# Performance work log

Measured on AMD Instinct MI355X. Metric: run time of the kernel, lower is better.

## Reference

```python
import jax, jax.numpy as jnp
import numpy as np

E, D, H, T = 8, 1024, 2816, 16384


def setup_inputs() -> dict:
    key = jax.random.key(0)
    k1, k2, k3, k4 = jax.random.split(key, 4)
    x = jax.random.normal(k1, (T, D), dtype=jnp.float32)
    # Params sized per init (w1/w3: [E, H, D], w2: [E, D, H]), trunc-normal-ish scale 0.02
    w1 = 0.02 * jax.random.normal(k2, (E, H, D), dtype=jnp.float32)
    w2 = 0.02 * jax.random.normal(k3, (E, D, H), dtype=jnp.float32)
    w3 = 0.02 * jax.random.normal(k4, (E, H, D), dtype=jnp.float32)
    # Per-expert token counts summing to < T (tail rows are padding, output zeros)
    rng = np.random.default_rng(0)
    props = rng.dirichlet(4.0 * np.ones(E))
    counts = np.floor(props * (T - 64)).astype(np.int32)
    num_tokens_per_expert = jnp.asarray(counts, dtype=jnp.int32)
    return {"x": x, "w1": w1, "w2": w2, "w3": w3,
            "num_tokens_per_expert": num_tokens_per_expert}


def reference(x, w1, w2, w3, num_tokens_per_expert):
    # Tokens are grouped contiguously by expert; grouped GEMM via lax.ragged_dot.
    g = num_tokens_per_expert.astype(jnp.int32)
    # rhs for ragged_dot must be [groups, k, n]
    h1 = jax.lax.ragged_dot(x, jnp.swapaxes(w1, 1, 2), g)   # [T, H] = x @ w1[e].T
    h3 = jax.lax.ragged_dot(x, jnp.swapaxes(w3, 1, 2), g)   # [T, H]
    h = jax.nn.silu(h1) * h3                                # SwiGLU
    out = jax.lax.ragged_dot(h, jnp.swapaxes(w2, 1, 2), g)  # [T, D]
    # Rows beyond sum(counts) are padding -> zeros, matching torch vstack of zeros
    valid = jnp.arange(x.shape[0]) < jnp.sum(g)
    return jnp.where(valid[:, None], out, jnp.zeros((), dtype=out.dtype))
```

## Files before the change

### kernel.cpp

```cpp
#include <hip/hip_runtime.h>

#define NE 8
#define DD 1024
#define HH 2816
#define TT 16384
#define MAX_TILES (TT / 128 + NE)

typedef __bf16 bf16;
typedef __bf16 bf16x4 __attribute__((ext_vector_type(4)));
typedef __bf16 bf16x8 __attribute__((ext_vector_type(8)));
typedef float f32x4 __attribute__((ext_vector_type(4)));

constexpr size_t HBUF_E = (size_t)TT * HH;
constexpr size_t XN = (size_t)TT * DD;
constexpr size_t WN = (size_t)NE * HH * DD;
constexpr size_t XB_OFF = HBUF_E * 2;
constexpr size_t W1B_OFF = XB_OFF + XN * 2;
constexpr size_t W3B_OFF = W1B_OFF + WN * 2;

__device__ __forceinline__ void gld16(const void* g, void* l) {
  __builtin_amdgcn_global_load_lds(
      (const __attribute__((address_space(1))) void*)g,
      (__attribute__((address_space(3))) void*)l, 16, 0, 0);
}

__device__ __forceinline__ f32x4 mfma16(bf16x8 a, bf16x8 b, f32x4 c) {
  return __builtin_amdgcn_mfma_f32_16x16x32_bf16(a, b, c, 0, 0, 0);
}

__global__ __launch_bounds__(256) void cvt_bf16_k(const float4* __restrict__ in,
                                                  bf16x4* __restrict__ out, int n4) {
  int i = blockIdx.x * 256 + threadIdx.x;
  if (i < n4) {
    float4 v = in[i];
    bf16x4 o;
    o[0] = (bf16)v.x; o[1] = (bf16)v.y; o[2] = (bf16)v.z; o[3] = (bf16)v.w;
    out[i] = o;
  }
}

struct TileInfo { int e, row0, rv; };
__device__ __forceinline__ TileInfo find_tile(const int* __restrict__ cnts, int t) {
  TileInfo ti; ti.e = -1; ti.row0 = 0; ti.rv = 0;
  int off = 0;
#pragma unroll
  for (int i = 0; i < NE; ++i) {
    int c = cnts[i];
    int tl = (c + 127) >> 7;
    if (ti.e < 0) {
      if (t < tl) {
        ti.e = i;
        ti.row0 = off + (t << 7);
        int rv = c - (t << 7);
        ti.rv = rv > 128 ? 128 : rv;
      } else {
        t -= tl;
      }
    }
    off += c;
  }
  return ti;
}

__global__ __launch_bounds__(256) void swiglu_gemm_k(
    const bf16* __restrict__ x, const bf16* __restrict__ w1,
    const bf16* __restrict__ w3, const int* __restrict__ cnts,
    bf16* __restrict__ hbuf) {
  constexpr int BK = 32;
  TileInfo ti = find_tile(cnts, blockIdx.x);
  if (ti.e < 0) return;
  const int n0 = blockIdx.y * 64;
  const bf16* w1e = w1 + (size_t)ti.e * HH * DD;
  const bf16* w3e = w3 + (size_t)ti.e * HH * DD;

  __shared__ bf16 lA[128 * BK];
  __shared__ bf16 lB1[64 * BK];
  __shared__ bf16 lB3[64 * BK];

  const int tid = threadIdx.x;
  const int wave = tid >> 6, lane = tid & 63;
  const int wm = wave >> 1, wn = wave & 1;
  const int lr = lane & 15, lk = (lane >> 4) << 3;

  const int rclamp = ti.rv - 1;
  int ar0 = tid >> 2;
  int ar1 = (256 + tid) >> 2;
  if (ar0 > rclamp) ar0 = rclamp;
  if (ar1 > rclamp) ar1 = rclamp;
  const int ac = (tid & 3) << 3;
  const int brow = tid >> 2;

  const bf16* xb = x + (size_t)ti.row0 * DD;

  f32x4 acc1[4][2], acc3[4][2];
#pragma unroll
  for (int i = 0; i < 4; ++i)
#pragma unroll
    for (int j = 0; j < 2; ++j) {
      acc1[i][j] = f32x4{0.f, 0.f, 0.f, 0.f};
      acc3[i][j] = f32x4{0.f, 0.f, 0.f, 0.f};
    }

  for (int k0 = 0; k0 < DD; k0 += BK) {
    gld16(xb + (size_t)ar0 * DD + k0 + ac, &lA[(size_t)tid * 8]);
    gld16(xb + (size_t)ar1 * DD + k0 + ac, &lA[(size_t)(256 + tid) * 8]);
    gld16(w1e + (size_t)(n0 + brow) * DD + k0 + ac, &lB1[(size_t)tid * 8]);
    gld16(w3e + (size_t)(n0 + brow) * DD + k0 + ac, &lB3[(size_t)tid * 8]);
    __syncthreads();

    bf16x8 af[4], b1f[2], b3f[2];
#pragma unroll
    for (int mt = 0; mt < 4; ++mt)
      af[mt] = *(const bf16x8*)&lA[(wm * 64 + mt * 16 + lr) * BK + lk];
#pragma unroll
    for (int nt = 0; nt < 2; ++nt) {
      b1f[nt] = *(const bf16x8*)&lB1[(wn * 32 + nt * 16 + lr) * BK + lk];
      b3f[nt] = *(const bf16x8*)&lB3[(wn * 32 + nt * 16 + lr) * BK + lk];
    }
#pragma unroll
    for (int mt = 0; mt < 4; ++mt)
#pragma unroll
      for (int nt = 0; nt < 2; ++nt) {
        acc1[mt][nt] = mfma16(af[mt], b1f[nt], acc1[mt][nt]);
        acc3[mt][nt] = mfma16(af[mt], b3f[nt], acc3[mt][nt]);
      }
    __syncthreads();
  }

  const int rquad = (lane >> 4) << 2;
#pragma unroll
  for (int mt = 0; mt < 4; ++mt) {
#pragma unroll
    for (int r = 0; r < 4; ++r) {
      int row = wm * 64 + mt * 16 + rquad + r;
      if (row < ti.rv) {
        size_t base = (size_t)(ti.row0 + row) * HH + n0 + wn * 32 + lr;
#pragma unroll
        for (int nt = 0; nt < 2; ++nt) {
          float a = acc1[mt][nt][r];
          float b = acc3[mt][nt][r];
          float s = a / (1.f + __expf(-a));
          hbuf[base + nt * 16] = (bf16)(s * b);
        }
      }
    }
  }
}

__global__ __launch_bounds__(256) void down_gemm_k(
    const bf16* __restrict__ hbuf, const bf16* __restrict__ w2,
    const int* __restrict__ cnts, float* __restrict__ out) {
  constexpr int BK = 32;
  TileInfo ti = find_tile(cnts, blockIdx.x);
  if (ti.e < 0) return;
  const int n0 = blockIdx.y * 128;
  const bf16* w2e = w2 + (size_t)ti.e * DD * HH;

  __shared__ bf16 lA[128 * BK];
  __shared__ bf16 lB[128 * BK];

  const int tid = threadIdx.x;
  const int wave = tid >> 6, lane = tid & 63;
  const int wm = wave >> 1, wn = wave & 1;
  const int lr = lane & 15, lk = (lane >> 4) << 3;

  const int rclamp = ti.rv - 1;
  int ar0 = tid >> 2;
  int ar1 = (256 + tid) >> 2;
  const int br0 = tid >> 2;
  const int br1 = (256 + tid) >> 2;
  if (ar0 > rclamp) ar0 = rclamp;
  if (ar1 > rclamp) ar1 = rclamp;
  const int ac = (tid & 3) << 3;

  const bf16* hb = hbuf + (size_t)ti.row0 * HH;

  f32x4 acc[4][4];
#pragma unroll
  for (int i = 0; i < 4; ++i)
#pragma unroll
    for (int j = 0; j < 4; ++j) acc[i][j] = f32x4{0.f, 0.f, 0.f, 0.f};

  for (int k0 = 0; k0 < HH; k0 += BK) {
    gld16(hb + (size_t)ar0 * HH + k0 + ac, &lA[(size_t)tid * 8]);
    gld16(hb + (size_t)ar1 * HH + k0 + ac, &lA[(size_t)(256 + tid) * 8]);
    gld16(w2e + (size_t)(n0 + br0) * HH + k0 + ac, &lB[(size_t)tid * 8]);
    gld16(w2e + (size_t)(n0 + br1) * HH + k0 + ac, &lB[(size_t)(256 + tid) * 8]);
    __syncthreads();

    bf16x8 af[4], bfm[4];
#pragma unroll
    for (int mt = 0; mt < 4; ++mt)
      af[mt] = *(const bf16x8*)&lA[(wm * 64 + mt * 16 + lr) * BK + lk];
#pragma unroll
    for (int nt = 0; nt < 4; ++nt)
      bfm[nt] = *(const bf16x8*)&lB[(wn * 64 + nt * 16 + lr) * BK + lk];
#pragma unroll
    for (int mt = 0; mt < 4; ++mt)
#pragma unroll
      for (int nt = 0; nt < 4; ++nt)
        acc[mt][nt] = mfma16(af[mt], bfm[nt], acc[mt][nt]);
    __syncthreads();
  }

  const int rquad = (lane >> 4) << 2;
#pragma unroll
  for (int mt = 0; mt < 4; ++mt) {
#pragma unroll
    for (int r = 0; r < 4; ++r) {
      int row = wm * 64 + mt * 16 + rquad + r;
      if (row < ti.rv) {
        size_t base = (size_t)(ti.row0 + row) * DD + n0 + wn * 64 + lr;
#pragma unroll
        for (int nt = 0; nt < 4; ++nt) out[base + nt * 16] = acc[mt][nt][r];
      }
    }
  }
}

extern "C" void kernel_launch(void* const* d_in, const int* in_sizes, int n_in,
                              void* d_out, int out_size, void* d_ws, size_t ws_size,
                              hipStream_t stream) {
  const float* x = (const float*)d_in[0];
  const float* w1 = (const float*)d_in[1];
  const float* w2 = (const float*)d_in[2];
  const float* w3 = (const float*)d_in[3];
  const int* cnts = (const int*)d_in[4];
  float* out = (float*)d_out;

  char* ws = (char*)d_ws;
  bf16* hbuf = (bf16*)ws;
  bf16* xb = (bf16*)(ws + XB_OFF);
  bf16* w1b = (bf16*)(ws + W1B_OFF);
  bf16* w3b = (bf16*)(ws + W3B_OFF);
  bf16* w2b = w1b;

  hipMemsetAsync(d_out, 0, (size_t)out_size * sizeof(float), stream);

  cvt_bf16_k<<<(int)(XN / 4 / 256), 256, 0, stream>>>((const float4*)x, (bf16x4*)xb, (int)(XN / 4));
  cvt_bf16_k<<<(int)(WN / 4 / 256), 256, 0, stream>>>((const float4*)w1, (bf16x4*)w1b, (int)(WN / 4));
  cvt_bf16_k<<<(int)(WN / 4 / 256), 256, 0, stream>>>((const float4*)w3, (bf16x4*)w3b, (int)(WN / 4));

  dim3 gA(MAX_TILES, HH / 64);
  swiglu_gemm_k<<<gA, 256, 0, stream>>>(xb, w1b, w3b, cnts, hbuf);

  cvt_bf16_k<<<(int)(WN / 4 / 256), 256, 0, stream>>>((const float4*)w2, (bf16x4*)w2b, (int)(WN / 4));

  dim3 gB(MAX_TILES, DD / 128);
  down_gemm_k<<<gB, 256, 0, stream>>>(hbuf, w2b, cnts, out);
}
```

Measured before the change: 780.6 us.

## Triple-buffer LDS pipeline with swizzled layout, larger tiles and XCD-aware block remap

Both grouped GEMM kernels now use 512-thread blocks with 128x128 output tiles and BK=64. The K loop is triple-buffered, with async global-to-LDS prefetch two stages ahead and explicit vmcnt waits in place of two syncthreads per iteration. LDS reads use an XOR swizzle to avoid bank conflicts, MFMA sections are raised in priority with setprio, and the 1D grid is remapped so consecutive blocks spread across the 8 XCDs. These changes target memory latency stalls and LDS bank conflicts. The cost is much larger shared-memory use (144KB for the swiglu kernel), which may limit occupancy or exceed the LDS budget.

```diff
diff --git a/kernel.cpp b/kernel.cpp
--- a/kernel.cpp
+++ b/kernel.cpp
@@ -4,7 +4,10 @@
 #define DD 1024
 #define HH 2816
 #define TT 16384
-#define MAX_TILES (TT / 128 + NE)
+#define MT (TT / 128 + NE)
+
+constexpr int NJA = MT * (HH / 128);
+constexpr int NJB = MT * (DD / 128);
 
 typedef __bf16 bf16;
 typedef __bf16 bf16x4 __attribute__((ext_vector_type(4)));
@@ -27,6 +30,12 @@
 __device__ __forceinline__ f32x4 mfma16(bf16x8 a, bf16x8 b, f32x4 c) {
   return __builtin_amdgcn_mfma_f32_16x16x32_bf16(a, b, c, 0, 0, 0);
 }
+
+#define BARRIER()                      \
+  do {                                 \
+    __builtin_amdgcn_s_barrier();      \
+    asm volatile("" ::: "memory");     \
+  } while (0)
 
 __global__ __launch_bounds__(256) void cvt_bf16_k(const float4* __restrict__ in,
                                                   bf16x4* __restrict__ out, int n4) {
@@ -62,35 +71,59 @@
   return ti;
 }
 
-__global__ __launch_bounds__(256) void swiglu_gemm_k(
+__global__ __launch_bounds__(512, 2) void swiglu_gemm_k(
     const bf16* __restrict__ x, const bf16* __restrict__ w1,
     const bf16* __restrict__ w3, const int* __restrict__ cnts,
     bf16* __restrict__ hbuf) {
-  constexpr int BK = 32;
-  TileInfo ti = find_tile(cnts, blockIdx.x);
+  constexpr int NKT = DD / 64;
+
+  int lin = blockIdx.x;
+  lin = (lin & 7) * (NJA / 8) + (lin >> 3);
+  const int tile = lin % MT;
+  const int n0 = (lin / MT) * 128;
+  TileInfo ti = find_tile(cnts, tile);
   if (ti.e < 0) return;
-  const int n0 = blockIdx.y * 64;
+
   const bf16* w1e = w1 + (size_t)ti.e * HH * DD;
   const bf16* w3e = w3 + (size_t)ti.e * HH * DD;
-
-  __shared__ bf16 lA[128 * BK];
-  __shared__ bf16 lB1[64 * BK];
-  __shared__ bf16 lB3[64 * BK];
+  const bf16* xb = x + (size_t)ti.row0 * DD;
+
+  __shared__ bf16 sA[3][128 * 64];
+  __shared__ bf16 sB1[3][128 * 64];
+  __shared__ bf16 sB3[3][128 * 64];
 
   const int tid = threadIdx.x;
-  const int wave = tid >> 6, lane = tid & 63;
-  const int wm = wave >> 1, wn = wave & 1;
-  const int lr = lane & 15, lk = (lane >> 4) << 3;
-
-  const int rclamp = ti.rv - 1;
-  int ar0 = tid >> 2;
-  int ar1 = (256 + tid) >> 2;
-  if (ar0 > rclamp) ar0 = rclamp;
-  if (ar1 > rclamp) ar1 = rclamp;
-  const int ac = (tid & 3) << 3;
-  const int brow = tid >> 2;
-
-  const bf16* xb = x + (size_t)ti.row0 * DD;
+  const int lane = tid & 63, wave = tid >> 6;
+  const int wm = wave >> 2, wn = wave & 3;
+  const int lr = lane & 15, lkg = lane >> 4;
+
+  const int r8 = tid >> 3;
+  const int csrc = ((tid & 7) ^ (r8 & 7)) << 3;
+  const int rvm1 = ti.rv - 1;
+  const int ra0 = r8 > rvm1 ? rvm1 : r8;
+  const int ra1 = (64 + r8) > rvm1 ? rvm1 : 64 + r8;
+  const bf16* gA0 = xb + (size_t)ra0 * DD + csrc;
+  const bf16* gA1 = xb + (size_t)ra1 * DD + csrc;
+  const bf16* gB1a = w1e + (size_t)(n0 + r8) * DD + csrc;
+  const bf16* gB1b = w1e + (size_t)(n0 + 64 + r8) * DD + csrc;
+  const bf16* gB3a = w3e + (size_t)(n0 + r8) * DD + csrc;
+  const bf16* gB3b = w3e + (size_t)(n0 + 64 + r8) * DD + csrc;
+  const int d0 = tid * 8, d1 = 64 * 64 + tid * 8;
+
+#define STAGE_A(kt, bb)                  \
+  do {                                   \
+    int kk = (kt) * 64;                  \
+    gld16(gA0 + kk, &sA[bb][d0]);        \
+    gld16(gA1 + kk, &sA[bb][d1]);        \
+    gld16(gB1a + kk, &sB1[bb][d0]);      \
+    gld16(gB1b + kk, &sB1[bb][d1]);      \
+    gld16(gB3a + kk, &sB3[bb][d0]);      \
+    gld16(gB3b + kk, &sB3[bb][d1]);      \
+  } while (0)
+
+  const int swz = (lkg ^ (lr & 7)) << 4;
+  const int aoff = (wm * 64 + lr) * 128 + swz;
+  const int boff = (wn * 32 + lr) * 128 + swz;
 
   f32x4 acc1[4][2], acc3[4][2];
 #pragma unroll
@@ -101,121 +134,173 @@
       acc3[i][j] = f32x4{0.f, 0.f, 0.f, 0.f};
     }
 
-  for (int k0 = 0; k0 < DD; k0 += BK) {
-    gld16(xb + (size_t)ar0 * DD + k0 + ac, &lA[(size_t)tid * 8]);
-    gld16(xb + (size_t)ar1 * DD + k0 + ac, &lA[(size_t)(256 + tid) * 8]);
-    gld16(w1e + (size_t)(n0 + brow) * DD + k0 + ac, &lB1[(size_t)tid * 8]);
-    gld16(w3e + (size_t)(n0 + brow) * DD + k0 + ac, &lB3[(size_t)tid * 8]);
-    __syncthreads();
-
-    bf16x8 af[4], b1f[2], b3f[2];
+  STAGE_A(0, 0);
+  STAGE_A(1, 1);
+  asm volatile("s_waitcnt vmcnt(6)" ::: "memory");
+  BARRIER();
+
+  int cur = 0;
+  for (int kt = 0; kt < NKT; ++kt) {
+    const bool pf = (kt + 2) < NKT;
+    int nxt = cur + 2; if (nxt >= 3) nxt -= 3;
+    if (pf) STAGE_A(kt + 2, nxt);
+
+    const char* pA = (const char*)sA[cur];
+    const char* pB1 = (const char*)sB1[cur];
+    const char* pB3 = (const char*)sB3[cur];
+    bf16x8 af[4][2], f1[2][2], f3[2][2];
 #pragma unroll
     for (int mt = 0; mt < 4; ++mt)
-      af[mt] = *(const bf16x8*)&lA[(wm * 64 + mt * 16 + lr) * BK + lk];
-#pragma unroll
-    for (int nt = 0; nt < 2; ++nt) {
-      b1f[nt] = *(const bf16x8*)&lB1[(wn * 32 + nt * 16 + lr) * BK + lk];
-      b3f[nt] = *(const bf16x8*)&lB3[(wn * 32 + nt * 16 + lr) * BK + lk];
-    }
-#pragma unroll
-    for (int mt = 0; mt < 4; ++mt)
-#pragma unroll
-      for (int nt = 0; nt < 2; ++nt) {
-        acc1[mt][nt] = mfma16(af[mt], b1f[nt], acc1[mt][nt]);
-        acc3[mt][nt] = mfma16(af[mt], b3f[nt], acc3[mt][nt]);
+#pragma unroll
+      for (int ks = 0; ks < 2; ++ks)
+        af[mt][ks] = *(const bf16x8*)(pA + ((aoff + mt * 2048) ^ (ks << 6)));
+#pragma unroll
+    for (int nt = 0; nt < 2; ++nt)
+#pragma unroll
+      for (int ks = 0; ks < 2; ++ks) {
+        f1[nt][ks] = *(const bf16x8*)(pB1 + ((boff + nt * 2048) ^ (ks << 6)));
+        f3[nt][ks] = *(const bf16x8*)(pB3 + ((boff + nt * 2048) ^ (ks << 6)));
       }
-    __syncthreads();
+    __builtin_amdgcn_s_setprio(1);
+#pragma unroll
+    for (int ks = 0; ks < 2; ++ks)
+#pragma unroll
+      for (int mt = 0; mt < 4; ++mt)
+#pragma unroll
+        for (int nt = 0; nt < 2; ++nt) {
+          acc1[mt][nt] = mfma16(af[mt][ks], f1[nt][ks], acc1[mt][nt]);
+          acc3[mt][nt] = mfma16(af[mt][ks], f3[nt][ks], acc3[mt][nt]);
+        }
+    __builtin_amdgcn_s_setprio(0);
+    if (pf) asm volatile("s_waitcnt vmcnt(6) lgkmcnt(0)" ::: "memory");
+    else    asm volatile("s_waitcnt vmcnt(0) lgkmcnt(0)" ::: "memory");
+    BARRIER();
+    cur = (cur + 1 == 3) ? 0 : cur + 1;
   }
-
-  const int rquad = (lane >> 4) << 2;
-#pragma unroll
-  for (int mt = 0; mt < 4; ++mt) {
+#undef STAGE_A
+
+  const int rq = (lane >> 4) << 2;
+#pragma unroll
+  for (int mt = 0; mt < 4; ++mt)
 #pragma unroll
     for (int r = 0; r < 4; ++r) {
-      int row = wm * 64 + mt * 16 + rquad + r;
+      int row = wm * 64 + mt * 16 + rq + r;
       if (row < ti.rv) {
         size_t base = (size_t)(ti.row0 + row) * HH + n0 + wn * 32 + lr;
 #pragma unroll
         for (int nt = 0; nt < 2; ++nt) {
-          float a = acc1[mt][nt][r];
-          float b = acc3[mt][nt][r];
-          float s = a / (1.f + __expf(-a));
-          hbuf[base + nt * 16] = (bf16)(s * b);
+          float a = acc1[mt][nt][r], b = acc3[mt][nt][r];
+          hbuf[base + nt * 16] = (bf16)(a / (1.f + __expf(-a)) * b);
         }
       }
     }
-  }
-}
-
-__global__ __launch_bounds__(256) void down_gemm_k(
+}
+
+__global__ __launch_bounds__(512, 2) void down_gemm_k(
     const bf16* __restrict__ hbuf, const bf16* __restrict__ w2,
     const int* __restrict__ cnts, float* __restrict__ out) {
-  constexpr int BK = 32;
-  TileInfo ti = find_tile(cnts, blockIdx.x);
+  constexpr int NKT = HH / 64;
+
+  int lin = blockIdx.x;
+  lin = (lin & 7) * (NJB / 8) + (lin >> 3);
+  const int tile = lin % MT;
+  const int n0 = (lin / MT) * 128;
+  TileInfo ti = find_tile(cnts, tile);
   if (ti.e < 0) return;
-  const int n0 = blockIdx.y * 128;
+
   const bf16* w2e = w2 + (size_t)ti.e * DD * HH;
-
-  __shared__ bf16 lA[128 * BK];
-  __shared__ bf16 lB[128 * BK];
+  const bf16* hb = hbuf + (size_t)ti.row0 * HH;
+
+  __shared__ bf16 sA[3][128 * 64];
+  __shared__ bf16 sB[3][128 * 64];
 
   const int tid = threadIdx.x;
-  const int wave = tid >> 6, lane = tid & 63;
-  const int wm = wave >> 1, wn = wave & 1;
-  const int lr = lane & 15, lk = (lane >> 4) << 3;
-
-  const int rclamp = ti.rv - 1;
-  int ar0 = tid >> 2;
-  int ar1 = (256 + tid) >> 2;
-  const int br0 = tid >> 2;
-  const int br1 = (256 + tid) >> 2;
-  if (ar0 > rclamp) ar0 = rclamp;
-  if (ar1 > rclamp) ar1 = rclamp;
-  const int ac = (tid & 3) << 3;
-
-  const bf16* hb = hbuf + (size_t)ti.row0 * HH;
-
-  f32x4 acc[4][4];
+  const int lane = tid & 63, wave = tid >> 6;
+  const int wm = wave >> 2, wn = wave & 3;
+  const int lr = lane & 15, lkg = lane >> 4;
+
+  const int r8 = tid >> 3;
+  const int csrc = ((tid & 7) ^ (r8 & 7)) << 3;
+  const int rvm1 = ti.rv - 1;
+  const int ra0 = r8 > rvm1 ? rvm1 : r8;
+  const int ra1 = (64 + r8) > rvm1 ? rvm1 : 64 + r8;
+  const bf16* gA0 = hb + (size_t)ra0 * HH + csrc;
+  const bf16* gA1 = hb + (size_t)ra1 * HH + csrc;
+  const bf16* gBa = w2e + (size_t)(n0 + r8) * HH + csrc;
+  const bf16* gBb = w2e + (size_t)(n0 + 64 + r8) * HH + csrc;
+  const int d0 = tid * 8, d1 = 64 * 64 + tid * 8;
+
+#define STAGE_B(kt, bb)                 \
+  do {                                  \
+    int kk = (kt) * 64;                 \
+    gld16(gA0 + kk, &sA[bb][d0]);       \
+    gld16(gA1 + kk, &sA[bb][d1]);       \
+    gld16(gBa + kk, &sB[bb][d0]);       \
+    gld16(gBb + kk, &sB[bb][d1]);       \
+  } while (0)
+
+  const int swz = (lkg ^ (lr & 7)) << 4;
+  const int aoff = (wm * 64 + lr) * 128 + swz;
+  const int boff = (wn * 32 + lr) * 128 + swz;
+
+  f32x4 acc[4][2];
 #pragma unroll
   for (int i = 0; i < 4; ++i)
 #pragma unroll
-    for (int j = 0; j < 4; ++j) acc[i][j] = f32x4{0.f, 0.f, 0.f, 0.f};
-
-  for (int k0 = 0; k0 < HH; k0 += BK) {
-    gld16(hb + (size_t)ar0 * HH + k0 + ac, &lA[(size_t)tid * 8]);
-    gld16(hb + (size_t)ar1 * HH + k0 + ac, &lA[(size_t)(256 + tid) * 8]);
-    gld16(w2e + (size_t)(n0 + br0) * HH + k0 + ac, &lB[(size_t)tid * 8]);
-    gld16(w2e + (size_t)(n0 + br1) * HH + k0 + ac, &lB[(size_t)(256 + tid) * 8]);
-    __syncthreads();
-
-    bf16x8 af[4], bfm[4];
+    for (int j = 0; j < 2; ++j) acc[i][j] = f32x4{0.f, 0.f, 0.f, 0.f};
+
+  STAGE_B(0, 0);
+  STAGE_B(1, 1);
+  asm volatile("s_waitcnt vmcnt(4)" ::: "memory");
+  BARRIER();
+
+  int cur = 0;
+  for (int kt = 0; kt < NKT; ++kt) {
+    const bool pf = (kt + 2) < NKT;
+    int nxt = cur + 2; if (nxt >= 3) nxt -= 3;
+    if (pf) STAGE_B(kt + 2, nxt);
+
+    const char* pA = (const char*)sA[cur];
+    const char* pB = (const char*)sB[cur];
+    bf16x8 af[4][2], bfm[2][2];
 #pragma unroll
     for (int mt = 0; mt < 4; ++mt)
-      af[mt] = *(const bf16x8*)&lA[(wm * 64 + mt * 16 + lr) * BK + lk];
-#pragma unroll
-    for (int nt = 0; nt < 4; ++nt)
-      bfm[nt] = *(const bf16x8*)&lB[(wn * 64 + nt * 16 + lr) * BK + lk];
-#pragma unroll
-    for (int mt = 0; mt < 4; ++mt)
-#pragma unroll
-      for (int nt = 0; nt < 4; ++nt)
-        acc[mt][nt] = mfma16(af[mt], bfm[nt], acc[mt][nt]);
-    __syncthreads();
+#pragma unroll
+      for (int ks = 0; ks < 2; ++ks)
+        af[mt][ks] = *(const bf16x8*)(pA + ((aoff + mt * 2048) ^ (ks << 6)));
+#pragma unroll
+    for (int nt = 0; nt < 2; ++nt)
+#pragma unroll
+      for (int ks = 0; ks < 2; ++ks)
+        bfm[nt][ks] = *(const bf16x8*)(pB + ((boff + nt * 2048) ^ (ks << 6)));
+    __builtin_amdgcn_s_setprio(1);
+#pragma unroll
+    for (int ks = 0; ks < 2; ++ks)
+#pragma unroll
+      for (int mt = 0; mt < 4; ++mt)
+#pragma unroll
+        for (int nt = 0; nt < 2; ++nt)
+          acc[mt][nt] = mfma16(af[mt][ks], bfm[nt][ks], acc[mt][nt]);
+    __builtin_amdgcn_s_setprio(0);
+    if (pf) asm volatile("s_waitcnt vmcnt(4) lgkmcnt(0)" ::: "memory");
+    else    asm volatile("s_waitcnt vmcnt(0) lgkmcnt(0)" ::: "memory");
+    BARRIER();
+    cur = (cur + 1 == 3) ? 0 : cur + 1;
   }
-
-  const int rquad = (lane >> 4) << 2;
-#pragma unroll
-  for (int mt = 0; mt < 4; ++mt) {
+#undef STAGE_B
+
+  const int rq = (lane >> 4) << 2;
+#pragma unroll
+  for (int mt = 0; mt < 4; ++mt)
 #pragma unroll
     for (int r = 0; r < 4; ++r) {
-      int row = wm * 64 + mt * 16 + rquad + r;
+      int row = wm * 64 + mt * 16 + rq + r;
       if (row < ti.rv) {
-        size_t base = (size_t)(ti.row0 + row) * DD + n0 + wn * 64 + lr;
-#pragma unroll
-        for (int nt = 0; nt < 4; ++nt) out[base + nt * 16] = acc[mt][nt][r];
+        size_t base = (size_t)(ti.row0 + row) * DD + n0 + wn * 32 + lr;
+#pragma unroll
+        for (int nt = 0; nt < 2; ++nt) out[base + nt * 16] = acc[mt][nt][r];
       }
     }
-  }
 }
 
 extern "C" void kernel_launch(void* const* d_in, const int* in_sizes, int n_in,
@@ -241,11 +326,9 @@
   cvt_bf16_k<<<(int)(WN / 4 / 256), 256, 0, stream>>>((const float4*)w1, (bf16x4*)w1b, (int)(WN / 4));
   cvt_bf16_k<<<(int)(WN / 4 / 256), 256, 0, stream>>>((const float4*)w3, (bf16x4*)w3b, (int)(WN / 4));
 
-  dim3 gA(MAX_TILES, HH / 64);
-  swiglu_gemm_k<<<gA, 256, 0, stream>>>(xb, w1b, w3b, cnts, hbuf);
+  swiglu_gemm_k<<<NJA, 512, 0, stream>>>(xb, w1b, w3b, cnts, hbuf);
 
   cvt_bf16_k<<<(int)(WN / 4 / 256), 256, 0, stream>>>((const float4*)w2, (bf16x4*)w2b, (int)(WN / 4));
 
-  dim3 gB(MAX_TILES, DD / 128);
-  down_gemm_k<<<gB, 256, 0, stream>>>(hbuf, w2b, cnts, out);
-}
+  down_gemm_k<<<NJB, 512, 0, stream>>>(hbuf, w2b, cnts, out);
+}
```

Result: slower. 888.2 us (+13.8%).
